# Kernel optimization log

Measured on AMD Instinct MI355X. Metric: run time of the kernel, lower is better.

Reference implementation:

```python
import jax, jax.numpy as jnp
import numpy as np

EPS = 1e-12  # torch F.normalize eps

def setup_inputs() -> dict:
    key = jax.random.key(0)
    k1, k2, k3, k4 = jax.random.split(key, 4)
    B, S, T, D, r = 8, 50, 77, 1024, 16
    h = jax.random.normal(k1, (B, S, T, D), dtype=jnp.float32)
    # R init: randn / sqrt(D), matching the torch module
    R = jax.random.normal(k2, (S, r, D), dtype=jnp.float32) / np.sqrt(D).astype(np.float32)
    # W, b are zero-init in the module; use small random values so the edit is non-trivial
    W = jax.random.normal(k3, (S, r, D), dtype=jnp.float32) * 0.02
    b = jax.random.normal(k4, (S, r), dtype=jnp.float32) * 0.02
    return {"h": h, "R": R, "W": W, "b": b}

def reference(h, R, W, b):
    # h: (B, S, T, D); R, W: (S, r, D); b: (S, r)
    # Per step t: Phi(h_t) = h_t + Rn_t^T (W_t h_t + b_t - Rn_t h_t), Rn = row-normalized R
    norm = jnp.sqrt(jnp.sum(R * R, axis=-1, keepdims=True))
    Rn = R / jnp.maximum(norm, EPS)
    Rh = jnp.einsum('bstd,srd->bstr', h, Rn)
    Wh = jnp.einsum('bstd,srd->bstr', h, W) + b[None, :, None, :]
    delta = jnp.einsum('bstr,srd->bstd', Wh - Rh, Rn)
    return h + delta
```

## Files before the change

kernel.cpp:

```cpp
#include <hip/hip_runtime.h>


typedef __attribute__((ext_vector_type(8))) short short8;
typedef __attribute__((ext_vector_type(4))) float floatx4;

__device__ __forceinline__ short f2bf(float f) {
  unsigned u = __float_as_uint(f);
  u += 0x7fffu + ((u >> 16) & 1u);
  return (short)(u >> 16);
}

#define S_ 50
#define T_ 77
#define NTOK 616

__global__ __launch_bounds__(256) void loreft_prep(
    const float* __restrict__ RG, const float* __restrict__ WG,
    short* __restrict__ Mg, short* __restrict__ Rg) {
  __shared__ float RnL[16][1024];
  const int s = blockIdx.x;
  const int tid = threadIdx.x;
  const int lane = tid & 63;
  const int wvi = tid >> 6;

#pragma unroll
  for (int rr = 0; rr < 4; ++rr) {
    const int r = wvi * 4 + rr;
    const floatx4* Rrow = (const floatx4*)(RG + (size_t)((s * 16 + r) << 10));
    const floatx4* Wrow = (const floatx4*)(WG + (size_t)((s * 16 + r) << 10));
    floatx4 rv0 = Rrow[lane * 4 + 0];
    floatx4 rv1 = Rrow[lane * 4 + 1];
    floatx4 rv2 = Rrow[lane * 4 + 2];
    floatx4 rv3 = Rrow[lane * 4 + 3];
    float ss = 0.f;
#pragma unroll
    for (int j = 0; j < 4; ++j)
      ss += rv0[j] * rv0[j] + rv1[j] * rv1[j] + rv2[j] * rv2[j] + rv3[j] * rv3[j];
#pragma unroll
    for (int m = 1; m < 64; m <<= 1) ss += __shfl_xor(ss, m);
    const float inv = 1.0f / fmaxf(sqrtf(ss), 1e-12f);

    floatx4 wa0 = Wrow[lane * 4 + 0];
    floatx4 wa1 = Wrow[lane * 4 + 1];
    floatx4 wa2 = Wrow[lane * 4 + 2];
    floatx4 wa3 = Wrow[lane * 4 + 3];
    float rn[16];
    short8 m0, m1;
#pragma unroll
    for (int j = 0; j < 4; ++j) {
      rn[j]      = rv0[j] * inv;  m0[j]     = f2bf(wa0[j] - rn[j]);
      rn[4 + j]  = rv1[j] * inv;  m0[4 + j] = f2bf(wa1[j] - rn[4 + j]);
      rn[8 + j]  = rv2[j] * inv;  m1[j]     = f2bf(wa2[j] - rn[8 + j]);
      rn[12 + j] = rv3[j] * inv;  m1[4 + j] = f2bf(wa3[j] - rn[12 + j]);
    }
    short* mdst = Mg + (size_t)(s * 16 + r) * 1024 + lane * 16;
    *(short8*)mdst = m0;
    *(short8*)(mdst + 8) = m1;
#pragma unroll
    for (int jj = 0; jj < 16; ++jj) RnL[r][lane * 16 + jj] = rn[jj];
  }
  __syncthreads();

#pragma unroll
  for (int dd = 0; dd < 4; ++dd) {
    const int d = dd * 256 + tid;
    short8 lo8, hi8;
#pragma unroll
    for (int rj = 0; rj < 8; ++rj) {
      lo8[rj] = f2bf(RnL[rj][d]);
      hi8[rj] = f2bf(RnL[rj + 8][d]);
    }
    short* dst = Rg + ((size_t)s * 1024 + d) * 16;
    *(short8*)dst = lo8;
    *(short8*)(dst + 8) = hi8;
  }
}

__global__ __launch_bounds__(128, 4) void loreft_main(
    const float* __restrict__ hG, const float* __restrict__ bG,
    const short* __restrict__ Mg, const short* __restrict__ Rg,
    float* __restrict__ outG) {
  const int tid = threadIdx.x;
  const int lane = tid & 63;
  const int wvi = tid >> 6;
  const int m16 = lane & 15;
  const int quad = lane >> 4;
  const int s = blockIdx.y;
  const int tile = blockIdx.x >> 1;
  const int half = blockIdx.x & 1;

  const int tokbase = tile * 16;
  int tokA = tokbase + m16; if (tokA > NTOK - 1) tokA = NTOK - 1;
  const int bb1 = tokA / T_;
  const int tt1 = tokA - bb1 * T_;
  const size_t rowoff = ((size_t)((bb1 * S_ + s) * T_ + tt1)) << 10;
  const float* hrow = hG + rowoff;
  const floatx4* hrow4 = (const floatx4*)hrow;
  const short* mrow = Mg + (size_t)(s * 16 + m16) * 1024 + quad * 8;

  floatx4 acc = {0.f, 0.f, 0.f, 0.f};
  floatx4 ha[4], hb[4];
  short8 mf[4];
#pragma unroll
  for (int j = 0; j < 4; ++j) {
    ha[j] = hrow4[j * 8 + quad * 2];
    hb[j] = hrow4[j * 8 + quad * 2 + 1];
    mf[j] = *(const short8*)(mrow + j * 32);
  }
#pragma unroll
  for (int g = 0; g < 8; ++g) {
    floatx4 na[4], nb[4];
    short8 nf[4];
    if (g < 7) {
#pragma unroll
      for (int j = 0; j < 4; ++j) {
        const int kb = (g + 1) * 4 + j;
        na[j] = hrow4[kb * 8 + quad * 2];
        nb[j] = hrow4[kb * 8 + quad * 2 + 1];
        nf[j] = *(const short8*)(mrow + kb * 32);
      }
    }
#pragma unroll
    for (int j = 0; j < 4; ++j) {
      short8 af;
#pragma unroll
      for (int i = 0; i < 4; ++i) { af[i] = f2bf(ha[j][i]); af[4 + i] = f2bf(hb[j][i]); }
      acc = __builtin_amdgcn_mfma_f32_16x16x32_bf16(af, mf[j], acc, 0, 0, 0);
    }
    if (g < 7) {
#pragma unroll
      for (int j = 0; j < 4; ++j) { ha[j] = na[j]; hb[j] = nb[j]; mf[j] = nf[j]; }
    }
  }

  const float bias = bG[s * 16 + m16];
  float cf[4];
#pragma unroll
  for (int i = 0; i < 4; ++i) cf[i] = acc[i] + bias;

  unsigned lo = ((unsigned)(unsigned short)f2bf(cf[0])) |
                (((unsigned)(unsigned short)f2bf(cf[1])) << 16);
  unsigned hi = ((unsigned)(unsigned short)f2bf(cf[2])) |
                (((unsigned)(unsigned short)f2bf(cf[3])) << 16);
  short8 bfrag;
  {
    const int srcbase = ((m16 >> 2) << 4) + ((quad & 1) << 3);
    const int regsel = m16 & 3;
#pragma unroll
    for (int j = 0; j < 8; ++j) {
      unsigned vlo = __shfl(lo, srcbase + j);
      unsigned vhi = __shfl(hi, srcbase + j);
      unsigned v32 = (regsel & 2) ? vhi : vlo;
      bfrag[j] = (short)((regsel & 1) ? (v32 >> 16) : (v32 & 0xffffu));
    }
  }
  const short8 zero8 = {0, 0, 0, 0, 0, 0, 0, 0};
  if (quad >= 2) bfrag = zero8;

  float* orow = outG + rowoff;
  const bool valE = (tokbase + m16) < NTOK;
  const int q16 = (quad & 1) << 3;
  const short* rbase = Rg + (size_t)s * (1024 * 16) + q16;
  const int dt0 = (half * 2 + wvi) * 16;

  short8 ar[4];
  floatx4 hv[4];
#pragma unroll
  for (int j = 0; j < 4; ++j) {
    const int dt = dt0 + j;
    ar[j] = (quad < 2) ? *(const short8*)(rbase + (dt * 16 + m16) * 16) : zero8;
    hv[j] = *(const floatx4*)(hrow + dt * 16 + quad * 4);
  }
#pragma unroll
  for (int g = 0; g < 4; ++g) {
    short8 nr[4];
    floatx4 nh[4];
    if (g < 3) {
#pragma unroll
      for (int j = 0; j < 4; ++j) {
        const int dt = dt0 + (g + 1) * 4 + j;
        nr[j] = (quad < 2) ? *(const short8*)(rbase + (dt * 16 + m16) * 16) : zero8;
        nh[j] = *(const floatx4*)(hrow + dt * 16 + quad * 4);
      }
    }
#pragma unroll
    for (int j = 0; j < 4; ++j) {
      const int dt = dt0 + g * 4 + j;
      floatx4 z = {0.f, 0.f, 0.f, 0.f};
      floatx4 dv = __builtin_amdgcn_mfma_f32_16x16x32_bf16(ar[j], bfrag, z, 0, 0, 0);
      if (valE) {
        floatx4 o;
#pragma unroll
        for (int i = 0; i < 4; ++i) o[i] = hv[j][i] + dv[i];
        *(floatx4*)(orow + dt * 16 + quad * 4) = o;
      }
    }
    if (g < 3) {
#pragma unroll
      for (int j = 0; j < 4; ++j) { ar[j] = nr[j]; hv[j] = nh[j]; }
    }
  }
}

extern "C" void kernel_launch(void* const* d_in, const int* in_sizes, int n_in,
                              void* d_out, int out_size, void* d_ws, size_t ws_size,
                              hipStream_t stream) {
  const float* h = (const float*)d_in[0];
  const float* R = (const float*)d_in[1];
  const float* W = (const float*)d_in[2];
  const float* b = (const float*)d_in[3];
  short* Mg = (short*)d_ws;
  short* Rg = Mg + (size_t)S_ * 16 * 1024;
  loreft_prep<<<dim3(S_), 256, 0, stream>>>(R, W, Mg, Rg);
  loreft_main<<<dim3(78, S_), 128, 0, stream>>>(h, b, Mg, Rg, (float*)d_out);
}
```

Before: 312.4 us.

## Stage each 16-token h tile in LDS once via direct global-to-LDS loads

The main kernel now loads each 16-token by 1024 h tile once into a 64KB XOR-swizzled LDS buffer using global_load_lds. Both the rank projection and the final residual add read h from LDS instead of re-reading it from global memory. The two half-blocks per tile are merged into one 256-thread block, and each wave redundantly computes the small projection and then writes a quarter of the output columns. This removes repeated HBM/L2 traffic on h, at the cost of higher LDS use per block, lower occupancy, and no overlap between the tile load and compute inside a block.

```diff
diff --git a/kernel.cpp b/kernel.cpp
--- a/kernel.cpp
+++ b/kernel.cpp
@@ -76,64 +76,71 @@
   }
 }
 
-__global__ __launch_bounds__(128, 4) void loreft_main(
+__global__ __launch_bounds__(256, 2) void loreft_main(
     const float* __restrict__ hG, const float* __restrict__ bG,
     const short* __restrict__ Mg, const short* __restrict__ Rg,
     float* __restrict__ outG) {
+  __shared__ float hT[16 * 1024];
+
   const int tid = threadIdx.x;
   const int lane = tid & 63;
   const int wvi = tid >> 6;
   const int m16 = lane & 15;
   const int quad = lane >> 4;
+  const int tile = blockIdx.x;
   const int s = blockIdx.y;
-  const int tile = blockIdx.x >> 1;
-  const int half = blockIdx.x & 1;
-
   const int tokbase = tile * 16;
+
+#pragma unroll
+  for (int rr = 0; rr < 4; ++rr) {
+    const int rloc = wvi * 4 + rr;
+    int tok = tokbase + rloc; if (tok > NTOK - 1) tok = NTOK - 1;
+    const int bb = tok / T_;
+    const int tt = tok - bb * T_;
+    const float* rsrc = hG + (((size_t)((bb * S_ + s) * T_ + tt)) << 10);
+    const int rsw = rloc & 7;
+    const int lsw = lane ^ rsw;
+#pragma unroll
+    for (int g = 0; g < 4; ++g) {
+      const float* gsrc = rsrc + ((g * 64 + lsw) << 2);
+      __builtin_amdgcn_global_load_lds(
+          (const __attribute__((address_space(1))) void*)gsrc,
+          (__attribute__((address_space(3))) void*)&hT[rloc * 1024 + g * 256],
+          16, 0, 0);
+    }
+  }
+
   int tokA = tokbase + m16; if (tokA > NTOK - 1) tokA = NTOK - 1;
   const int bb1 = tokA / T_;
   const int tt1 = tokA - bb1 * T_;
   const size_t rowoff = ((size_t)((bb1 * S_ + s) * T_ + tt1)) << 10;
-  const float* hrow = hG + rowoff;
-  const floatx4* hrow4 = (const floatx4*)hrow;
   const short* mrow = Mg + (size_t)(s * 16 + m16) * 1024 + quad * 8;
+  const float bias = bG[s * 16 + m16];
+  const int sw = m16 & 7;
+  const float* hls = &hT[m16 * 1024];
+
+  __syncthreads();
 
   floatx4 acc = {0.f, 0.f, 0.f, 0.f};
-  floatx4 ha[4], hb[4];
-  short8 mf[4];
-#pragma unroll
-  for (int j = 0; j < 4; ++j) {
-    ha[j] = hrow4[j * 8 + quad * 2];
-    hb[j] = hrow4[j * 8 + quad * 2 + 1];
-    mf[j] = *(const short8*)(mrow + j * 32);
-  }
-#pragma unroll
-  for (int g = 0; g < 8; ++g) {
-    floatx4 na[4], nb[4];
-    short8 nf[4];
-    if (g < 7) {
-#pragma unroll
-      for (int j = 0; j < 4; ++j) {
-        const int kb = (g + 1) * 4 + j;
-        na[j] = hrow4[kb * 8 + quad * 2];
-        nb[j] = hrow4[kb * 8 + quad * 2 + 1];
-        nf[j] = *(const short8*)(mrow + kb * 32);
-      }
-    }
-#pragma unroll
-    for (int j = 0; j < 4; ++j) {
+#pragma unroll
+  for (int kg = 0; kg < 4; ++kg) {
+    short8 mf[8];
+#pragma unroll
+    for (int j = 0; j < 8; ++j)
+      mf[j] = *(const short8*)(mrow + (kg * 8 + j) * 32);
+#pragma unroll
+    for (int j = 0; j < 8; ++j) {
+      const int kb = kg * 8 + j;
+      const int blk = kb * 8 + quad * 2;
+      floatx4 p0 = *(const floatx4*)(hls + (((blk) ^ sw) << 2));
+      floatx4 p1 = *(const floatx4*)(hls + (((blk + 1) ^ sw) << 2));
       short8 af;
 #pragma unroll
-      for (int i = 0; i < 4; ++i) { af[i] = f2bf(ha[j][i]); af[4 + i] = f2bf(hb[j][i]); }
+      for (int i = 0; i < 4; ++i) { af[i] = f2bf(p0[i]); af[4 + i] = f2bf(p1[i]); }
       acc = __builtin_amdgcn_mfma_f32_16x16x32_bf16(af, mf[j], acc, 0, 0, 0);
     }
-    if (g < 7) {
-#pragma unroll
-      for (int j = 0; j < 4; ++j) { ha[j] = na[j]; hb[j] = nb[j]; mf[j] = nf[j]; }
-    }
-  }
-
-  const float bias = bG[s * 16 + m16];
+  }
+
   float cf[4];
 #pragma unroll
   for (int i = 0; i < 4; ++i) cf[i] = acc[i] + bias;
@@ -161,26 +168,22 @@
   const bool valE = (tokbase + m16) < NTOK;
   const int q16 = (quad & 1) << 3;
   const short* rbase = Rg + (size_t)s * (1024 * 16) + q16;
-  const int dt0 = (half * 2 + wvi) * 16;
+  const int dt0 = wvi * 16;
 
   short8 ar[4];
-  floatx4 hv[4];
 #pragma unroll
   for (int j = 0; j < 4; ++j) {
     const int dt = dt0 + j;
     ar[j] = (quad < 2) ? *(const short8*)(rbase + (dt * 16 + m16) * 16) : zero8;
-    hv[j] = *(const floatx4*)(hrow + dt * 16 + quad * 4);
   }
 #pragma unroll
   for (int g = 0; g < 4; ++g) {
     short8 nr[4];
-    floatx4 nh[4];
     if (g < 3) {
 #pragma unroll
       for (int j = 0; j < 4; ++j) {
         const int dt = dt0 + (g + 1) * 4 + j;
         nr[j] = (quad < 2) ? *(const short8*)(rbase + (dt * 16 + m16) * 16) : zero8;
-        nh[j] = *(const floatx4*)(hrow + dt * 16 + quad * 4);
       }
     }
 #pragma unroll
@@ -188,16 +191,17 @@
       const int dt = dt0 + g * 4 + j;
       floatx4 z = {0.f, 0.f, 0.f, 0.f};
       floatx4 dv = __builtin_amdgcn_mfma_f32_16x16x32_bf16(ar[j], bfrag, z, 0, 0, 0);
+      floatx4 hv = *(const floatx4*)(&hT[m16 * 1024 + (((dt * 4 + quad) ^ sw) << 2)]);
       if (valE) {
         floatx4 o;
 #pragma unroll
-        for (int i = 0; i < 4; ++i) o[i] = hv[j][i] + dv[i];
+        for (int i = 0; i < 4; ++i) o[i] = hv[i] + dv[i];
         *(floatx4*)(orow + dt * 16 + quad * 4) = o;
       }
     }
     if (g < 3) {
 #pragma unroll
-      for (int j = 0; j < 4; ++j) { ar[j] = nr[j]; hv[j] = nh[j]; }
+      for (int j = 0; j < 4; ++j) ar[j] = nr[j];
     }
   }
 }
@@ -212,5 +216,5 @@
   short* Mg = (short*)d_ws;
   short* Rg = Mg + (size_t)S_ * 16 * 1024;
   loreft_prep<<<dim3(S_), 256, 0, stream>>>(R, W, Mg, Rg);
-  loreft_main<<<dim3(78, S_), 128, 0, stream>>>(h, b, Mg, Rg, (float*)d_out);
-}
+  loreft_main<<<dim3(39, S_), 256, 0, stream>>>(h, b, Mg, Rg, (float*)d_out);
+}
```

Result: faster. 263.2 us (-15.7%).
